# Kernel optimization log

Hardware: AMD Instinct MI355X
Metric: run time of the kernel (lower is better)

## Reference

```python
import jax, jax.numpy as jnp
import numpy as np

N = 50000      # nodes
E = 800000     # edges
T_MAX = 128
N_T = 128
NF = T_MAX * 3 # 384 node features


def setup_inputs() -> dict:
    key = jax.random.key(0)
    ks = jax.random.split(key, 12)
    def lin(k, fi, fo):
        k1, k2 = jax.random.split(k)
        s = 1.0 / np.sqrt(fi)
        return (jax.random.uniform(k1, (fi, fo), jnp.float32, -s, s),
                jax.random.uniform(k2, (fo,), jnp.float32, -s, s))
    x = jax.random.normal(ks[0], (N, NF), jnp.float32)
    edge_index = jax.random.randint(ks[1], (2, E), 0, N, jnp.int32)
    W1, b1 = lin(ks[2], NF, N_T)
    W2, b2 = lin(ks[3], N_T, N_T * 3)
    W3, b3 = lin(ks[4], N_T * 3, N_T * 2)
    W4, b4 = lin(ks[5], N_T * 2, NF)
    Wl, bl = lin(ks[6], NF, T_MAX)
    return {"x": x, "edge_index": edge_index,
            "W1": W1, "b1": b1, "W2": W2, "b2": b2,
            "W3": W3, "b3": b3, "W4": W4, "b4": b4,
            "Wl": Wl, "bl": bl}


def reference(x, edge_index, W1, b1, W2, b2, W3, b3, W4, b4, Wl, bl):
    # GCNConv (PyG defaults): add self-loops, symmetric normalization
    loop = jnp.arange(N, dtype=edge_index.dtype)
    src = jnp.concatenate([edge_index[0], loop])
    dst = jnp.concatenate([edge_index[1], loop])
    deg = jax.ops.segment_sum(jnp.ones_like(src, jnp.float32), dst, num_segments=N)
    dinv = jax.lax.rsqrt(deg)  # deg >= 1 due to self-loops
    norm = (dinv[src] * dinv[dst])[:, None]  # [E+N, 1]

    def gcn(h, W, b):
        hw = h @ W                       # [N, out]
        msg = hw[src] * norm             # gather + scale per edge
        agg = jax.ops.segment_sum(msg, dst, num_segments=N)
        return agg + b

    # dropout is identity in eval mode
    h = jax.nn.leaky_relu(gcn(x, W1, b1))
    h = jax.nn.leaky_relu(gcn(h, W2, b2))
    h = jax.nn.leaky_relu(gcn(h, W3, b3))
    h = jax.nn.leaky_relu(gcn(h, W4, b4))
    h = h @ Wl + bl
    return jax.nn.relu(h)  # args.schedule_deviation == False
```

## Files before the change

kernel.cpp:

```cpp
#include <hip/hip_runtime.h>

#define NNODES 50000
#define NEDGES 800000
#define NTILES ((NNODES + 255) / 256)
#define XFEAT (NNODES * 384)
#define XPREP_BLOCKS (XFEAT / (256 * 8))
#define WPREP_TOTAL 344064
#define WPREP_BLOCKS (WPREP_TOTAL / 256)

typedef unsigned short ushort_t;
typedef __attribute__((ext_vector_type(8))) short short8;
typedef __attribute__((ext_vector_type(4))) float floatx4;

__device__ __forceinline__ float bf2f(unsigned short u) {
  union { unsigned int i; float f; } v; v.i = ((unsigned int)u) << 16; return v.f;
}
__device__ __forceinline__ unsigned short f2bf(float f) {
  union { float f; unsigned int i; } v; v.f = f;
  unsigned int r = v.i + 0x7fffu + ((v.i >> 16) & 1u);
  return (unsigned short)(r >> 16);
}

__device__ __forceinline__ void gload_lds16(const void* g, void* l) {
  __builtin_amdgcn_global_load_lds(
      (const __attribute__((address_space(1))) unsigned int*)g,
      (__attribute__((address_space(3))) unsigned int*)l, 16, 0, 0);
}


__global__ void hist_kernel(const int* dst, int* cnt) {
  int i = blockIdx.x * 256 + threadIdx.x;
  if (i < NEDGES) atomicAdd(&cnt[dst[i]], 1);
}


__global__ __launch_bounds__(256) void tile_scan_kernel(
    const int* __restrict__ cnt, int* __restrict__ tile_pref, int* __restrict__ tile_sum) {
  __shared__ int s[256];
  int b = blockIdx.x, t = threadIdx.x;
  int i = b * 256 + t;
  int v = (i < NNODES) ? cnt[i] : 0;
  s[t] = v;
  __syncthreads();
#pragma unroll
  for (int off = 1; off < 256; off <<= 1) {
    int x = (t >= off) ? s[t - off] : 0;
    __syncthreads();
    s[t] += x;
    __syncthreads();
  }
  if (i < NNODES) tile_pref[i] = s[t] - v;
  if (t == 255) tile_sum[b] = s[255];
}

__global__ __launch_bounds__(256) void sum_scan_kernel(
    const int* __restrict__ tile_sum, int* __restrict__ tile_base) {
  __shared__ int s[256];
  int t = threadIdx.x;
  int v = (t < NTILES) ? tile_sum[t] : 0;
  s[t] = v;
  __syncthreads();
#pragma unroll
  for (int off = 1; off < 256; off <<= 1) {
    int x = (t >= off) ? s[t - off] : 0;
    __syncthreads();
    s[t] += x;
    __syncthreads();
  }
  if (t < NTILES) tile_base[t] = s[t] - v;
}

__global__ __launch_bounds__(256) void scan_write_kernel(
    const int* __restrict__ cnt, const int* __restrict__ tile_pref,
    const int* __restrict__ tile_base, int* __restrict__ row_ptr,
    int* __restrict__ cursor, float* __restrict__ dinv) {
  int b = blockIdx.x, t = threadIdx.x;
  int i = b * 256 + t;
  if (i < NNODES) {
    int base = tile_base[b] + tile_pref[i];
    row_ptr[i] = base;
    cursor[i] = base;
    dinv[i] = rsqrtf((float)(cnt[i] + 1));
    if (i == NNODES - 1) row_ptr[NNODES] = base + cnt[i];
  }
}

__global__ void fill_kernel(const int* src, const int* dst, int* cursor, int* col_idx) {
  int i = blockIdx.x * 256 + threadIdx.x;
  if (i < NEDGES) {
    int p = atomicAdd(&cursor[dst[i]], 1);
    col_idx[p] = src[i];
  }
}

__global__ __launch_bounds__(256) void prep_all(
    const float* __restrict__ x, ushort_t* __restrict__ xbf,
    const float* __restrict__ W1, ushort_t* __restrict__ W1h, ushort_t* __restrict__ W1l,
    const float* __restrict__ W2, ushort_t* __restrict__ W2h, ushort_t* __restrict__ W2l,
    const float* __restrict__ W3, ushort_t* __restrict__ W3h, ushort_t* __restrict__ W3l,
    const float* __restrict__ W4, ushort_t* __restrict__ W4h, ushort_t* __restrict__ W4l,
    const float* __restrict__ Wl, ushort_t* __restrict__ Wlh, ushort_t* __restrict__ Wll) {
  int b = blockIdx.x;
  if (b < XPREP_BLOCKS) {
    size_t i = ((size_t)b * 256 + threadIdx.x) * 8;
    float4 p0 = *(const float4*)(x + i);
    float4 p1 = *(const float4*)(x + i + 4);
    uint4 u;
    u.x = (unsigned int)f2bf(p0.x) | ((unsigned int)f2bf(p0.y) << 16);
    u.y = (unsigned int)f2bf(p0.z) | ((unsigned int)f2bf(p0.w) << 16);
    u.z = (unsigned int)f2bf(p1.x) | ((unsigned int)f2bf(p1.y) << 16);
    u.w = (unsigned int)f2bf(p1.z) | ((unsigned int)f2bf(p1.w) << 16);
    *(uint4*)(xbf + i) = u;
    return;
  }
  int t = (b - XPREP_BLOCKS) * 256 + threadIdx.x;
  const float* W; ushort_t* hi; ushort_t* lo; int K, N;
  if (t < 49152)       { W = W1; hi = W1h; lo = W1l; K = 384; N = 128; }
  else if (t < 98304)  { W = W2; hi = W2h; lo = W2l; K = 128; N = 384; t -= 49152; }
  else if (t < 196608) { W = W3; hi = W3h; lo = W3l; K = 384; N = 256; t -= 98304; }
  else if (t < 294912) { W = W4; hi = W4h; lo = W4l; K = 256; N = 384; t -= 196608; }
  else                 { W = Wl; hi = Wlh; lo = Wll; K = 384; N = 128; t -= 294912; }
  int n = t / K, k = t - n * K;
  float w = W[(size_t)k * N + n];
  unsigned short h = f2bf(w);
  hi[t] = h;
  lo[t] = f2bf(w - bf2f(h));
}


template <int WPL>
__device__ __forceinline__ void load_row(const ushort_t* p, float* f) {
  if (WPL == 2) {
    unsigned int u = *(const unsigned int*)p;
    f[0] = bf2f((unsigned short)(u & 0xffff));
    f[1] = bf2f((unsigned short)(u >> 16));
  } else {
    uint2 u = *(const uint2*)p;
    f[0] = bf2f((unsigned short)(u.x & 0xffff));
    f[1] = bf2f((unsigned short)(u.x >> 16));
    f[2] = bf2f((unsigned short)(u.y & 0xffff));
    f[3] = bf2f((unsigned short)(u.y >> 16));
  }
}

template <int WPL>
__global__ __launch_bounds__(256) void agg_kernel(
    const ushort_t* __restrict__ in, ushort_t* __restrict__ out,
    const int* __restrict__ row_ptr, const int* __restrict__ col_idx,
    const float* __restrict__ dinv, const float* __restrict__ bias,
    int mode, int scale_store) {
  const int W = WPL * 64;
  int wid = __builtin_amdgcn_readfirstlane(blockIdx.x * 4 + (int)(threadIdx.x >> 6));
  int lane = threadIdx.x & 63;
  int co = lane * WPL;
  const ushort_t* base = in + co;
  float acc[WPL];
  {
    float v[WPL];
    load_row<WPL>(base + (size_t)wid * W, v);
#pragma unroll
    for (int c = 0; c < WPL; ++c) acc[c] = v[c];
  }
  int e = row_ptr[wid], e1 = row_ptr[wid + 1];
  for (; e + 16 <= e1; e += 16) {
    int j[16];
#pragma unroll
    for (int q = 0; q < 16; ++q) j[q] = col_idx[e + q];
    float v[16][WPL];
#pragma unroll
    for (int q = 0; q < 16; ++q) load_row<WPL>(base + (size_t)j[q] * W, v[q]);
#pragma unroll
    for (int c = 0; c < WPL; ++c) {
      float s0 = (v[0][c] + v[1][c]) + (v[2][c] + v[3][c]);
      float s1 = (v[4][c] + v[5][c]) + (v[6][c] + v[7][c]);
      float s2 = (v[8][c] + v[9][c]) + (v[10][c] + v[11][c]);
      float s3 = (v[12][c] + v[13][c]) + (v[14][c] + v[15][c]);
      acc[c] += (s0 + s1) + (s2 + s3);
    }
  }
  for (; e + 4 <= e1; e += 4) {
    int j0 = col_idx[e], j1 = col_idx[e + 1], j2 = col_idx[e + 2], j3 = col_idx[e + 3];
    float v0[WPL], v1[WPL], v2[WPL], v3[WPL];
    load_row<WPL>(base + (size_t)j0 * W, v0);
    load_row<WPL>(base + (size_t)j1 * W, v1);
    load_row<WPL>(base + (size_t)j2 * W, v2);
    load_row<WPL>(base + (size_t)j3 * W, v3);
#pragma unroll
    for (int c = 0; c < WPL; ++c) acc[c] += (v0[c] + v1[c]) + (v2[c] + v3[c]);
  }
  for (; e < e1; ++e) {
    int j = col_idx[e];
    float v[WPL];
    load_row<WPL>(base + (size_t)j * W, v);
#pragma unroll
    for (int c = 0; c < WPL; ++c) acc[c] += v[c];
  }
  float di = dinv[wid];
  unsigned short o[WPL];
  if (mode) {
    float bb[WPL];
    if constexpr (WPL == 2) {
      float2 b2 = *(const float2*)(bias + co); bb[0] = b2.x; bb[1] = b2.y;
    } else {
      float4 b4 = *(const float4*)(bias + co);
      bb[0] = b4.x; bb[1] = b4.y; bb[2] = b4.z; bb[3] = b4.w;
    }
    float sc = scale_store ? di : 1.f;
#pragma unroll
    for (int c = 0; c < WPL; ++c) {
      float v = acc[c] * di + bb[c];
      v = v > 0.f ? v : 0.01f * v;
      o[c] = f2bf(v * sc);
    }
  } else {
#pragma unroll
    for (int c = 0; c < WPL; ++c) o[c] = f2bf(acc[c] * di);
  }
  if constexpr (WPL == 2) {
    *(unsigned int*)(out + (size_t)wid * W + co) =
        (unsigned int)o[0] | ((unsigned int)o[1] << 16);
  } else {
    uint2 u;
    u.x = (unsigned int)o[0] | ((unsigned int)o[1] << 16);
    u.y = (unsigned int)o[2] | ((unsigned int)o[3] << 16);
    *(uint2*)(out + (size_t)wid * W + co) = u;
  }
}


#define BK 32

template <int TBM, int TBN>
__global__ __launch_bounds__(256, TBM == 64 ? 6 : 4) void gemm_mfma(
    const ushort_t* __restrict__ A, const ushort_t* __restrict__ Bhi,
    const ushort_t* __restrict__ Blo, void* __restrict__ Cv,
    const float* __restrict__ bias, const float* __restrict__ dinv,
    int M, int K, int ldc, int mode, int scale_store, int out_f32) {
  constexpr int FR = TBM / 32;
  constexpr int FG = TBN / 32;
  constexpr int AIT = TBM / 64;
  constexpr int BIT = TBN / 64;
  __shared__ ushort_t As[TBM * BK];
  __shared__ ushort_t Bh[TBN * BK];
  __shared__ ushort_t Bl[TBN * BK];
  int tid = threadIdx.x;
  int lane = tid & 63, w = tid >> 6;
  int wm = w & 1, wn = w >> 1;
  int m0 = blockIdx.x * TBM, n0 = blockIdx.y * TBN;
  floatx4 acc[FR][FG] = {};
  int nkt = K / BK;
  for (int kt = 0; kt < nkt; ++kt) {
    int kb = kt * BK;
    __syncthreads();
#pragma unroll
    for (int it = 0; it < AIT; ++it) {
      int s = it * 256 + tid;
      int row = s >> 2, ks = (s & 3) * 8;
      int gr = m0 + row; if (gr > M - 1) gr = M - 1;
      gload_lds16(A + (size_t)gr * K + kb + ks,
                  As + (size_t)(it * 256 + w * 64) * 8);
    }
#pragma unroll
    for (int it = 0; it < BIT; ++it) {
      int s = it * 256 + tid;
      int row = s >> 2, ks = (s & 3) * 8;
      gload_lds16(Bhi + (size_t)(n0 + row) * K + kb + ks,
                  Bh + (size_t)(it * 256 + w * 64) * 8);
      gload_lds16(Blo + (size_t)(n0 + row) * K + kb + ks,
                  Bl + (size_t)(it * 256 + w * 64) * 8);
    }
    __syncthreads();
    short8 af[FR], fh[FG], fl[FG];
#pragma unroll
    for (int f = 0; f < FR; ++f)
      af[f] = *(const short8*)&As[(wm * (TBM / 2) + f * 16 + (lane & 15)) * BK + (lane >> 4) * 8];
#pragma unroll
    for (int g = 0; g < FG; ++g) {
      int o = (wn * (TBN / 2) + g * 16 + (lane & 15)) * BK + (lane >> 4) * 8;
      fh[g] = *(const short8*)&Bh[o];
      fl[g] = *(const short8*)&Bl[o];
    }
#pragma unroll
    for (int f = 0; f < FR; ++f)
#pragma unroll
      for (int g = 0; g < FG; ++g) {
        acc[f][g] = __builtin_amdgcn_mfma_f32_16x16x32_bf16(af[f], fh[g], acc[f][g], 0, 0, 0);
        acc[f][g] = __builtin_amdgcn_mfma_f32_16x16x32_bf16(af[f], fl[g], acc[f][g], 0, 0, 0);
      }
  }
  int cr = lane >> 4, cc = lane & 15;
#pragma unroll
  for (int f = 0; f < FR; ++f) {
#pragma unroll
    for (int r = 0; r < 4; ++r) {
      int row = m0 + wm * (TBM / 2) + f * 16 + cr * 4 + r;
      if (row >= M) continue;
      float sc = scale_store ? dinv[row] : 1.f;
#pragma unroll
      for (int g = 0; g < FG; ++g) {
        int col = n0 + wn * (TBN / 2) + g * 16 + cc;
        float v = acc[f][g][r];
        if (mode) {
          v += bias[col];
          v = (mode == 1) ? (v > 0.f ? v : 0.01f * v) : (v > 0.f ? v : 0.f);
        }
        v *= sc;
        if (out_f32) ((float*)Cv)[(size_t)row * ldc + col] = v;
        else ((ushort_t*)Cv)[(size_t)row * ldc + col] = f2bf(v);
      }
    }
  }
}


extern "C" void kernel_launch(void* const* d_in, const int* in_sizes, int n_in,
                              void* d_out, int out_size, void* d_ws, size_t ws_size,
                              hipStream_t stream) {
  const float* x  = (const float*)d_in[0];
  const int* ei   = (const int*)d_in[1];
  const float* W1 = (const float*)d_in[2];
  const float* b1 = (const float*)d_in[3];
  const float* W2 = (const float*)d_in[4];
  const float* b2 = (const float*)d_in[5];
  const float* W3 = (const float*)d_in[6];
  const float* b3 = (const float*)d_in[7];
  const float* W4 = (const float*)d_in[8];
  const float* b4 = (const float*)d_in[9];
  const float* Wl = (const float*)d_in[10];
  const float* bl = (const float*)d_in[11];

  char* p = (char*)d_ws;
  auto alloc = [&](size_t bytes) {
    char* r = p;
    p += (bytes + 255) & ~(size_t)255;
    return r;
  };
  int* cnt       = (int*)alloc((size_t)NNODES * 4);
  int* cursor    = (int*)alloc((size_t)NNODES * 4);
  int* row_ptr   = (int*)alloc((size_t)(NNODES + 1) * 4);
  float* dinv    = (float*)alloc((size_t)NNODES * 4);
  int* col_idx   = (int*)alloc((size_t)NEDGES * 4);
  int* tile_pref = (int*)alloc((size_t)NNODES * 4);
  int* tile_sum  = (int*)alloc(256 * 4);
  int* tile_base = (int*)alloc(256 * 4);
  ushort_t* W1h = (ushort_t*)alloc(49152 * 2); ushort_t* W1l = (ushort_t*)alloc(49152 * 2);
  ushort_t* W2h = (ushort_t*)alloc(49152 * 2); ushort_t* W2l = (ushort_t*)alloc(49152 * 2);
  ushort_t* W3h = (ushort_t*)alloc(98304 * 2); ushort_t* W3l = (ushort_t*)alloc(98304 * 2);
  ushort_t* W4h = (ushort_t*)alloc(98304 * 2); ushort_t* W4l = (ushort_t*)alloc(98304 * 2);
  ushort_t* Wlh = (ushort_t*)alloc(49152 * 2); ushort_t* Wll = (ushort_t*)alloc(49152 * 2);
  ushort_t* actA = (ushort_t*)alloc((size_t)NNODES * 384 * 2);
  ushort_t* actB = (ushort_t*)alloc((size_t)NNODES * 384 * 2);
  ushort_t* xbf = actB;

  const int* src = ei;
  const int* dst = ei + NEDGES;

  hipMemsetAsync(cnt, 0, (size_t)NNODES * 4, stream);
  hist_kernel<<<(NEDGES + 255) / 256, 256, 0, stream>>>(dst, cnt);
  tile_scan_kernel<<<NTILES, 256, 0, stream>>>(cnt, tile_pref, tile_sum);
  sum_scan_kernel<<<1, 256, 0, stream>>>(tile_sum, tile_base);
  scan_write_kernel<<<NTILES, 256, 0, stream>>>(cnt, tile_pref, tile_base, row_ptr, cursor, dinv);
  fill_kernel<<<(NEDGES + 255) / 256, 256, 0, stream>>>(src, dst, cursor, col_idx);

  prep_all<<<XPREP_BLOCKS + WPREP_BLOCKS, 256, 0, stream>>>(
      x, xbf, W1, W1h, W1l, W2, W2h, W2l, W3, W3h, W3l, W4, W4h, W4l, Wl, Wlh, Wll);

  dim3 blk(256);
  int gm64  = (NNODES + 63) / 64;
  int gm128 = (NNODES + 127) / 128;
  int nagg = NNODES / 4;

  gemm_mfma<64, 64><<<dim3(gm64, 2), blk, 0, stream>>>(xbf, W1h, W1l, actA, (const float*)0, dinv, NNODES, 384, 128, 0, 1, 0);
  agg_kernel<2><<<nagg, blk, 0, stream>>>(actA, actB, row_ptr, col_idx, dinv, b1, 1, 1);
  agg_kernel<2><<<nagg, blk, 0, stream>>>(actB, actA, row_ptr, col_idx, dinv, (const float*)0, 0, 0);
  gemm_mfma<128, 128><<<dim3(gm128, 3), blk, 0, stream>>>(actA, W2h, W2l, actB, b2, dinv, NNODES, 128, 384, 1, 0, 0);
  gemm_mfma<128, 128><<<dim3(gm128, 2), blk, 0, stream>>>(actB, W3h, W3l, actA, (const float*)0, dinv, NNODES, 384, 256, 0, 1, 0);
  agg_kernel<4><<<nagg, blk, 0, stream>>>(actA, actB, row_ptr, col_idx, dinv, b3, 1, 1);
  agg_kernel<4><<<nagg, blk, 0, stream>>>(actB, actA, row_ptr, col_idx, dinv, (const float*)0, 0, 0);
  gemm_mfma<128, 128><<<dim3(gm128, 3), blk, 0, stream>>>(actA, W4h, W4l, actB, b4, dinv, NNODES, 256, 384, 1, 0, 0);
  gemm_mfma<64, 64><<<dim3(gm64, 2), blk, 0, stream>>>(actB, Wlh, Wll, d_out, bl, dinv, NNODES, 384, 128, 2, 0, 1);
}
```

Measured before the change: 580.0 us.

## Split aggregation feature columns into halves and process four nodes per wave

The aggregation kernel now splits each node's feature row into two column halves handled by separate blocks. Pairs of consecutive block groups cover the two halves of the same node range, so the gathered rows are probably meant to share L2 residency. Each wave now loops over four nodes instead of one, with the bias loaded once per wave. The goal is a smaller per-pass gather footprint and better cache locality, at the cost of narrower per-lane loads (one or two bf16 per lane) and twice as many index loads.

Measured after the change: 588.0 us. Within noise of the previous version (+1.4%).

```diff
diff --git a/kernel.cpp b/kernel.cpp
--- a/kernel.cpp
+++ b/kernel.cpp
@@ -128,102 +128,98 @@
 }
 
 
-template <int WPL>
-__device__ __forceinline__ void load_row(const ushort_t* p, float* f) {
-  if (WPL == 2) {
+template <int WH>
+__device__ __forceinline__ void load_rowh(const ushort_t* p, float* f) {
+  if (WH == 1) {
+    f[0] = bf2f(*p);
+  } else {
     unsigned int u = *(const unsigned int*)p;
     f[0] = bf2f((unsigned short)(u & 0xffff));
     f[1] = bf2f((unsigned short)(u >> 16));
-  } else {
-    uint2 u = *(const uint2*)p;
-    f[0] = bf2f((unsigned short)(u.x & 0xffff));
-    f[1] = bf2f((unsigned short)(u.x >> 16));
-    f[2] = bf2f((unsigned short)(u.y & 0xffff));
-    f[3] = bf2f((unsigned short)(u.y >> 16));
-  }
-}
-
-template <int WPL>
+  }
+}
+
+template <int C>
 __global__ __launch_bounds__(256) void agg_kernel(
     const ushort_t* __restrict__ in, ushort_t* __restrict__ out,
     const int* __restrict__ row_ptr, const int* __restrict__ col_idx,
     const float* __restrict__ dinv, const float* __restrict__ bias,
     int mode, int scale_store) {
-  const int W = WPL * 64;
-  int wid = __builtin_amdgcn_readfirstlane(blockIdx.x * 4 + (int)(threadIdx.x >> 6));
+  constexpr int WH = C / 128;
+  int b = blockIdx.x;
+  int half = (b >> 2) & 1;
+  int idx = (b >> 3) * 4 + (b & 3);
+  if (idx >= 3125) return;
+  int wave = idx * 4 + (int)(threadIdx.x >> 6);
   int lane = threadIdx.x & 63;
-  int co = lane * WPL;
+  int co = half * (C / 2) + lane * WH;
   const ushort_t* base = in + co;
-  float acc[WPL];
-  {
-    float v[WPL];
-    load_row<WPL>(base + (size_t)wid * W, v);
-#pragma unroll
-    for (int c = 0; c < WPL; ++c) acc[c] = v[c];
-  }
-  int e = row_ptr[wid], e1 = row_ptr[wid + 1];
-  for (; e + 16 <= e1; e += 16) {
-    int j[16];
-#pragma unroll
-    for (int q = 0; q < 16; ++q) j[q] = col_idx[e + q];
-    float v[16][WPL];
-#pragma unroll
-    for (int q = 0; q < 16; ++q) load_row<WPL>(base + (size_t)j[q] * W, v[q]);
-#pragma unroll
-    for (int c = 0; c < WPL; ++c) {
-      float s0 = (v[0][c] + v[1][c]) + (v[2][c] + v[3][c]);
-      float s1 = (v[4][c] + v[5][c]) + (v[6][c] + v[7][c]);
-      float s2 = (v[8][c] + v[9][c]) + (v[10][c] + v[11][c]);
-      float s3 = (v[12][c] + v[13][c]) + (v[14][c] + v[15][c]);
-      acc[c] += (s0 + s1) + (s2 + s3);
-    }
-  }
-  for (; e + 4 <= e1; e += 4) {
-    int j0 = col_idx[e], j1 = col_idx[e + 1], j2 = col_idx[e + 2], j3 = col_idx[e + 3];
-    float v0[WPL], v1[WPL], v2[WPL], v3[WPL];
-    load_row<WPL>(base + (size_t)j0 * W, v0);
-    load_row<WPL>(base + (size_t)j1 * W, v1);
-    load_row<WPL>(base + (size_t)j2 * W, v2);
-    load_row<WPL>(base + (size_t)j3 * W, v3);
-#pragma unroll
-    for (int c = 0; c < WPL; ++c) acc[c] += (v0[c] + v1[c]) + (v2[c] + v3[c]);
-  }
-  for (; e < e1; ++e) {
-    int j = col_idx[e];
-    float v[WPL];
-    load_row<WPL>(base + (size_t)j * W, v);
-#pragma unroll
-    for (int c = 0; c < WPL; ++c) acc[c] += v[c];
-  }
-  float di = dinv[wid];
-  unsigned short o[WPL];
+  float bb[WH];
   if (mode) {
-    float bb[WPL];
-    if constexpr (WPL == 2) {
-      float2 b2 = *(const float2*)(bias + co); bb[0] = b2.x; bb[1] = b2.y;
+    if (WH == 1) {
+      bb[0] = bias[co];
     } else {
-      float4 b4 = *(const float4*)(bias + co);
-      bb[0] = b4.x; bb[1] = b4.y; bb[2] = b4.z; bb[3] = b4.w;
-    }
-    float sc = scale_store ? di : 1.f;
-#pragma unroll
-    for (int c = 0; c < WPL; ++c) {
-      float v = acc[c] * di + bb[c];
-      v = v > 0.f ? v : 0.01f * v;
-      o[c] = f2bf(v * sc);
-    }
-  } else {
-#pragma unroll
-    for (int c = 0; c < WPL; ++c) o[c] = f2bf(acc[c] * di);
-  }
-  if constexpr (WPL == 2) {
-    *(unsigned int*)(out + (size_t)wid * W + co) =
-        (unsigned int)o[0] | ((unsigned int)o[1] << 16);
-  } else {
-    uint2 u;
-    u.x = (unsigned int)o[0] | ((unsigned int)o[1] << 16);
-    u.y = (unsigned int)o[2] | ((unsigned int)o[3] << 16);
-    *(uint2*)(out + (size_t)wid * W + co) = u;
+      float2 b2 = *(const float2*)(bias + co);
+      bb[0] = b2.x; bb[1] = b2.y;
+    }
+  }
+  for (int k = 0; k < 4; ++k) {
+    int wid = __builtin_amdgcn_readfirstlane(wave * 4 + k);
+    float acc[WH];
+    load_rowh<WH>(base + (size_t)wid * C, acc);
+    int e = row_ptr[wid], e1 = row_ptr[wid + 1];
+    for (; e + 16 <= e1; e += 16) {
+      int j[16];
+#pragma unroll
+      for (int q = 0; q < 16; ++q) j[q] = col_idx[e + q];
+      float v[16][WH];
+#pragma unroll
+      for (int q = 0; q < 16; ++q) load_rowh<WH>(base + (size_t)j[q] * C, v[q]);
+#pragma unroll
+      for (int c = 0; c < WH; ++c) {
+        float s0 = (v[0][c] + v[1][c]) + (v[2][c] + v[3][c]);
+        float s1 = (v[4][c] + v[5][c]) + (v[6][c] + v[7][c]);
+        float s2 = (v[8][c] + v[9][c]) + (v[10][c] + v[11][c]);
+        float s3 = (v[12][c] + v[13][c]) + (v[14][c] + v[15][c]);
+        acc[c] += (s0 + s1) + (s2 + s3);
+      }
+    }
+    for (; e + 4 <= e1; e += 4) {
+      int j0 = col_idx[e], j1 = col_idx[e + 1], j2 = col_idx[e + 2], j3 = col_idx[e + 3];
+      float v0[WH], v1[WH], v2[WH], v3[WH];
+      load_rowh<WH>(base + (size_t)j0 * C, v0);
+      load_rowh<WH>(base + (size_t)j1 * C, v1);
+      load_rowh<WH>(base + (size_t)j2 * C, v2);
+      load_rowh<WH>(base + (size_t)j3 * C, v3);
+#pragma unroll
+      for (int c = 0; c < WH; ++c) acc[c] += (v0[c] + v1[c]) + (v2[c] + v3[c]);
+    }
+    for (; e < e1; ++e) {
+      int j = col_idx[e];
+      float v[WH];
+      load_rowh<WH>(base + (size_t)j * C, v);
+#pragma unroll
+      for (int c = 0; c < WH; ++c) acc[c] += v[c];
+    }
+    float di = dinv[wid];
+    if (mode) {
+      float sc = scale_store ? di : 1.f;
+#pragma unroll
+      for (int c = 0; c < WH; ++c) {
+        float v = acc[c] * di + bb[c];
+        v = v > 0.f ? v : 0.01f * v;
+        acc[c] = v * sc;
+      }
+    } else {
+#pragma unroll
+      for (int c = 0; c < WH; ++c) acc[c] *= di;
+    }
+    if (WH == 1) {
+      out[(size_t)wid * C + co] = f2bf(acc[0]);
+    } else {
+      *(unsigned int*)(out + (size_t)wid * C + co) =
+          (unsigned int)f2bf(acc[0]) | ((unsigned int)f2bf(acc[1]) << 16);
+    }
   }
 }
 
@@ -368,15 +364,15 @@
   dim3 blk(256);
   int gm64  = (NNODES + 63) / 64;
   int gm128 = (NNODES + 127) / 128;
-  int nagg = NNODES / 4;
+  int gagg  = 6256;
 
   gemm_mfma<64, 64><<<dim3(gm64, 2), blk, 0, stream>>>(xbf, W1h, W1l, actA, (const float*)0, dinv, NNODES, 384, 128, 0, 1, 0);
-  agg_kernel<2><<<nagg, blk, 0, stream>>>(actA, actB, row_ptr, col_idx, dinv, b1, 1, 1);
-  agg_kernel<2><<<nagg, blk, 0, stream>>>(actB, actA, row_ptr, col_idx, dinv, (const float*)0, 0, 0);
+  agg_kernel<128><<<gagg, blk, 0, stream>>>(actA, actB, row_ptr, col_idx, dinv, b1, 1, 1);
+  agg_kernel<128><<<gagg, blk, 0, stream>>>(actB, actA, row_ptr, col_idx, dinv, (const float*)0, 0, 0);
   gemm_mfma<128, 128><<<dim3(gm128, 3), blk, 0, stream>>>(actA, W2h, W2l, actB, b2, dinv, NNODES, 128, 384, 1, 0, 0);
   gemm_mfma<128, 128><<<dim3(gm128, 2), blk, 0, stream>>>(actB, W3h, W3l, actA, (const float*)0, dinv, NNODES, 384, 256, 0, 1, 0);
-  agg_kernel<4><<<nagg, blk, 0, stream>>>(actA, actB, row_ptr, col_idx, dinv, b3, 1, 1);
-  agg_kernel<4><<<nagg, blk, 0, stream>>>(actB, actA, row_ptr, col_idx, dinv, (const float*)0, 0, 0);
+  agg_kernel<256><<<gagg, blk, 0, stream>>>(actA, actB, row_ptr, col_idx, dinv, b3, 1, 1);
+  agg_kernel<256><<<gagg, blk, 0, stream>>>(actB, actA, row_ptr, col_idx, dinv, (const float*)0, 0, 0);
   gemm_mfma<128, 128><<<dim3(gm128, 3), blk, 0, stream>>>(actA, W4h, W4l, actB, b4, dinv, NNODES, 256, 384, 1, 0, 0);
   gemm_mfma<64, 64><<<dim3(gm64, 2), blk, 0, stream>>>(actB, Wlh, Wll, d_out, bl, dinv, NNODES, 384, 128, 2, 0, 1);
 }
```
